# Kernel tuning notes

Hardware: AMD Instinct MI355X
Metric: run time of the kernel (lower is better)

Reference implementation:

```python
import jax, jax.numpy as jnp
import numpy as np

B, L, D = 8, 2048, 1024

def setup_inputs() -> dict:
    key = jax.random.key(0)
    ks = jax.random.split(key, 4)
    s = 1.0 / np.sqrt(D)  # linear init scale
    x = jax.random.normal(ks[0], (B, L, D), dtype=jnp.float32)
    mask = jnp.zeros((B, L, L), dtype=jnp.float32)  # additive attention mask
    Wq = jax.random.normal(ks[1], (D, D), dtype=jnp.float32) * s
    Wk = jax.random.normal(ks[2], (D, D), dtype=jnp.float32) * s
    Wv = jax.random.normal(ks[3], (D, D), dtype=jnp.float32) * s
    bq = jnp.zeros((D,), dtype=jnp.float32)
    bk = jnp.zeros((D,), dtype=jnp.float32)
    bv = jnp.zeros((D,), dtype=jnp.float32)
    return {"x": x, "mask": mask, "Wq": Wq, "bq": bq, "Wk": Wk, "bk": bk, "Wv": Wv, "bv": bv}

def reference(x, mask, Wq, bq, Wk, bk, Wv, bv):
    # Linear projections (torch Linear: y = x @ W.T + b)
    q = jnp.einsum('bld,ed->ble', x, Wq) + bq
    k = jnp.einsum('bld,ed->ble', x, Wk) + bk
    v = jnp.einsum('bld,ed->ble', x, Wv) + bv
    d = x.shape[2]
    logits = jnp.einsum('bqd,bkd->bqk', q, k) / jnp.sqrt(jnp.float32(d))
    probas = jax.nn.softmax(logits + mask, axis=2)
    return jnp.einsum('bqk,bkd->bqd', probas, v)
```

## Files before the change

### kernel.cpp

```cpp
#include <hip/hip_runtime.h>
#include <hip/hip_bf16.h>
#include <hip/hip_fp16.h>

typedef __attribute__((ext_vector_type(8))) short short8;
typedef __attribute__((ext_vector_type(4))) short sh4;
typedef __attribute__((ext_vector_type(8))) _Float16 half8;
typedef __attribute__((ext_vector_type(4))) float floatx4;

__device__ __forceinline__ unsigned short f2bf(float f) {
    unsigned int u = __builtin_bit_cast(unsigned int, f);
    u += 0x7fffu + ((u >> 16) & 1u);
    return (unsigned short)(u >> 16);
}

__device__ __forceinline__ void gl_lds16(const unsigned short* g, unsigned short* l) {
    __builtin_amdgcn_global_load_lds(
        (const __attribute__((address_space(1))) unsigned int*)(const void*)g,
        (__attribute__((address_space(3))) unsigned int*)(void*)l,
        16, 0, 0);
}

#define BM 256
#define BN 256
#define BK 64

template<int OMODE>
__global__ __launch_bounds__(512, 2)
void gemm_bt(const unsigned short* __restrict__ A,
             const unsigned short* __restrict__ B,
             void* __restrict__ O,
             const float* __restrict__ bias0, const float* __restrict__ bias1,
             const float* __restrict__ bias2,
             int K, int lda, int ldb, int ldo,
             long long aBS, long long bBS, long long oBS,
             float scale, int nby, int vstart,
             unsigned short* __restrict__ Vt, int ldvt)
{
    __shared__ __align__(16) unsigned short lds[2][2][BM * BK];

    const int t = threadIdx.x;
    const int lane = t & 63;
    const int w = t >> 6;
    const int wr = w >> 2;
    const int wc = w & 3;
    const int lq = lane >> 4;
    const int lr = lane & 15;

    const int nwg = gridDim.x;
    const int swz = (blockIdx.x & 7) * (nwg >> 3) + (blockIdx.x >> 3);
    const int by = swz % nby, bx = swz / nby;
    const size_t m0 = (size_t)bx * BM, n0 = (size_t)by * BN;

    const int z = blockIdx.z;
    const unsigned short* Az = A + (size_t)z * aBS;
    const unsigned short* Bz = B + (size_t)z * bBS;

    const int srow = t >> 3;
    const int scol = ((t & 7) ^ (srow & 7)) << 3;

    floatx4 acc[8][4];
#pragma unroll
    for (int i = 0; i < 8; ++i)
#pragma unroll
        for (int j = 0; j < 4; ++j)
            acc[i][j] = (floatx4){0.f, 0.f, 0.f, 0.f};

    const int NT = K / BK;

    auto stage = [&](int mat, int u, int kt, int buf) {
        const unsigned short* g = (mat ? Bz + (n0 + u * 64 + srow) * (size_t)ldb
                                       : Az + (m0 + u * 64 + srow) * (size_t)lda) + kt + scol;
        gl_lds16(g, &lds[buf][mat][u * 4096 + w * 512]);
    };

#pragma unroll
    for (int u = 0; u < 4; ++u) stage(1, u, 0, 0);
#pragma unroll
    for (int u = 0; u < 4; ++u) stage(0, u, 0, 0);
    if (NT > 1) {
#pragma unroll
        for (int u = 0; u < 4; ++u) stage(1, u, BK, 1);
        asm volatile("s_waitcnt vmcnt(4)" ::: "memory");
    } else {
        asm volatile("s_waitcnt vmcnt(0)" ::: "memory");
    }
    __builtin_amdgcn_s_barrier();
    __builtin_amdgcn_sched_barrier(0);

    for (int tt = 0; tt < NT; ++tt) {
        const int cur = tt & 1, nxt = cur ^ 1;
        const int kt1 = (tt + 1) * BK, kt2 = (tt + 2) * BK;
        short8 bfr[4][2];
#pragma unroll
        for (int p = 0; p < 4; ++p) {
            short8 af[2][2];
            if (p == 0) {
#pragma unroll
                for (int ni = 0; ni < 4; ++ni)
#pragma unroll
                    for (int kk = 0; kk < 2; ++kk) {
                        const int rb = wc * 64 + ni * 16 + lr;
                        const int j = kk * 4 + lq;
                        bfr[ni][kk] = *(const short8*)&lds[cur][1][rb * 64 + ((j ^ (rb & 7)) << 3)];
                    }
            }
#pragma unroll
            for (int mi2 = 0; mi2 < 2; ++mi2)
#pragma unroll
                for (int kk = 0; kk < 2; ++kk) {
                    const int ra = wr * 128 + (2 * p + mi2) * 16 + lr;
                    const int j = kk * 4 + lq;
                    af[mi2][kk] = *(const short8*)&lds[cur][0][ra * 64 + ((j ^ (ra & 7)) << 3)];
                }
            if (p == 0 && tt + 1 < NT) { stage(0, 0, kt1, nxt); stage(0, 1, kt1, nxt); }
            if (p == 1 && tt + 1 < NT) { stage(0, 2, kt1, nxt); stage(0, 3, kt1, nxt); }
            if (p == 2 && tt + 2 < NT) { stage(1, 0, kt2, cur); stage(1, 1, kt2, cur); }
            if (p == 3 && tt + 2 < NT) { stage(1, 2, kt2, cur); stage(1, 3, kt2, cur); }

            __builtin_amdgcn_sched_barrier(0);
            __builtin_amdgcn_s_barrier();
            __builtin_amdgcn_sched_barrier(0);
            __builtin_amdgcn_s_setprio(1);
#pragma unroll
            for (int kk = 0; kk < 2; ++kk)
#pragma unroll
                for (int mi2 = 0; mi2 < 2; ++mi2)
#pragma unroll
                    for (int ni = 0; ni < 4; ++ni)
                        acc[2 * p + mi2][ni] = __builtin_amdgcn_mfma_f32_16x16x32_bf16(
                            af[mi2][kk], bfr[ni][kk], acc[2 * p + mi2][ni], 0, 0, 0);
            __builtin_amdgcn_s_setprio(0);
            __builtin_amdgcn_sched_barrier(0);
            if (p == 3) {
                if (tt < NT - 2) asm volatile("s_waitcnt vmcnt(4)" ::: "memory");
                else             asm volatile("s_waitcnt vmcnt(0)" ::: "memory");
            }
            __builtin_amdgcn_s_barrier();
            __builtin_amdgcn_sched_barrier(0);
        }
    }

    const float* bias = bias0; int cshift = 0;
    if (bias1) {
        const int r = (int)(n0 >> 10);
        bias = (r == 0) ? bias0 : ((r == 1) ? bias1 : bias2);
        cshift = r << 10;
    }

    if (vstart >= 0 && (int)n0 >= vstart) {
        unsigned short* lf = &lds[0][0][0] + w * 8192;
        __syncthreads();
#pragma unroll
        for (int mi = 0; mi < 8; ++mi) {
#pragma unroll
            for (int ni = 0; ni < 4; ++ni) {
                const int tc = ni * 16 + lr;
                const int col = (int)n0 + wc * 64 + tc;
                const float cb = bias ? bias[col - cshift] : 0.f;
                const int tr0 = mi * 16 + lq * 4;
                floatx4 v = acc[mi][ni];
                sh4 pk;
#pragma unroll
                for (int r = 0; r < 4; ++r) pk[r] = (short)f2bf(v[r] * scale + cb);
                *(sh4*)&lf[tc * 128 + (tr0 ^ ((tc & 7) << 3))] = pk;
            }
        }
        __syncthreads();
        const int vrow_base = (int)n0 - vstart + wc * 64;
        const size_t colb = m0 + (size_t)wr * 128 + (size_t)(lane & 15) * 8;
#pragma unroll
        for (int i = 0; i < 16; ++i) {
            const int vr = i * 4 + (lane >> 4);
            short8 d = *(const short8*)&lf[vr * 128 + (((lane & 15) * 8) ^ ((vr & 7) << 3))];
            *(short8*)&Vt[(size_t)(vrow_base + vr) * ldvt + colb] = d;
        }
    } else {
#pragma unroll
        for (int mi = 0; mi < 8; ++mi) {
#pragma unroll
            for (int ni = 0; ni < 4; ++ni) {
                const size_t col = n0 + wc * 64 + ni * 16 + lr;
                const float cb = bias ? bias[col - cshift] : 0.f;
                floatx4 v = acc[mi][ni];
#pragma unroll
                for (int r = 0; r < 4; ++r) {
                    const size_t row = m0 + wr * 128 + mi * 16 + lq * 4 + r;
                    const float val = v[r] * scale + cb;
                    const size_t off = (size_t)z * oBS + row * (size_t)ldo + col;
                    if (OMODE == 0)
                        ((unsigned short*)O)[off] = f2bf(val);
                    else if (OMODE == 1)
                        ((float*)O)[off] = val;
                    else {
                        _Float16 h = (_Float16)val;
                        ((unsigned short*)O)[off] = __builtin_bit_cast(unsigned short, h);
                    }
                }
            }
        }
    }
}

__global__ void cvt4(const float4* __restrict__ s0, ushort4* __restrict__ d0, int n0,
                     const float4* __restrict__ s1, ushort4* __restrict__ d1, int n1,
                     const float4* __restrict__ s2, ushort4* __restrict__ d2, int n2,
                     const float4* __restrict__ s3, ushort4* __restrict__ d3, int n3)
{
    const int total = n0 + n1 + n2 + n3;
    const int stride = gridDim.x * blockDim.x;
    for (int i = blockIdx.x * blockDim.x + threadIdx.x; i < total; i += stride) {
        const float4* s; ushort4* d; int j = i;
        if (j < n0) { s = s0; d = d0; }
        else { j -= n0;
            if (j < n1) { s = s1; d = d1; }
            else { j -= n1;
                if (j < n2) { s = s2; d = d2; }
                else { j -= n2; s = s3; d = d3; }
            }
        }
        float4 f = s[j];
        d[j] = (ushort4){f2bf(f.x), f2bf(f.y), f2bf(f.z), f2bf(f.w)};
    }
}

__global__ void softmax_kernel(_Float16* __restrict__ S, const float* __restrict__ mask, int b0)
{
    const int lane = threadIdx.x & 63;
    const int wid = threadIdx.x >> 6;
    const size_t rowid = (size_t)blockIdx.x * 4 + wid;
    const size_t bi = rowid >> 11;
    const size_t q = rowid & 2047;
    _Float16* Srow = S + rowid * 2048;
    const float* Mrow = mask + (((size_t)b0 + bi) * 2048 + q) * 2048;

    float v[32];
    float mx = -3.4e38f;
#pragma unroll
    for (int i = 0; i < 4; ++i) {
        half8 h = ((const half8*)Srow)[i * 64 + lane];
        float4 ma = ((const float4*)Mrow)[i * 128 + lane * 2];
        float4 mb = ((const float4*)Mrow)[i * 128 + lane * 2 + 1];
        const float* mp0 = (const float*)&ma;
        const float* mp1 = (const float*)&mb;
#pragma unroll
        for (int j = 0; j < 4; ++j) {
            v[i * 8 + j]     = (float)h[j]     + mp0[j];
            v[i * 8 + 4 + j] = (float)h[4 + j] + mp1[j];
        }
#pragma unroll
        for (int j = 0; j < 8; ++j) mx = fmaxf(mx, v[i * 8 + j]);
    }
#pragma unroll
    for (int off = 32; off; off >>= 1) mx = fmaxf(mx, __shfl_xor(mx, off, 64));
    float sum = 0.f;
#pragma unroll
    for (int i = 0; i < 32; ++i) { v[i] = __expf(v[i] - mx); sum += v[i]; }
#pragma unroll
    for (int off = 32; off; off >>= 1) sum += __shfl_xor(sum, off, 64);
    const float inv = 1.0f / sum;

    unsigned short* Prow = (unsigned short*)Srow;
#pragma unroll
    for (int i = 0; i < 4; ++i) {
        short8 pk;
#pragma unroll
        for (int j = 0; j < 8; ++j) pk[j] = (short)f2bf(v[i * 8 + j] * inv);
        ((short8*)Prow)[i * 64 + lane] = pk;
    }
}

extern "C" void kernel_launch(void* const* d_in, const int* in_sizes, int n_in,
                              void* d_out, int out_size, void* d_ws, size_t ws_size,
                              hipStream_t stream)
{
    const float* x    = (const float*)d_in[0];
    const float* mask = (const float*)d_in[1];
    const float* Wq   = (const float*)d_in[2];
    const float* bq   = (const float*)d_in[3];
    const float* Wk   = (const float*)d_in[4];
    const float* bk   = (const float*)d_in[5];
    const float* Wv   = (const float*)d_in[6];
    const float* bv   = (const float*)d_in[7];
    float* out = (float*)d_out;

    const size_t MB = 1ull << 20;
    char* ws = (char*)d_ws;
    unsigned short* QKb  = (unsigned short*)(ws);
    unsigned short* Vt   = (unsigned short*)(ws + 64 * MB);
    unsigned short* Wcat = (unsigned short*)(ws + 96 * MB);
    unsigned short* xb   = (unsigned short*)(ws + 102 * MB);
    _Float16* Sb         = (_Float16*)(ws + 134 * MB);

    size_t savail = (ws_size > 134 * MB) ? ws_size - 134 * MB : 0;
    int g = (int)(savail / (8 * MB));
    if (g < 1) g = 1;
    if (g > 8) g = 8;

    cvt4<<<2048, 256, 0, stream>>>(
        (const float4*)x,  (ushort4*)xb,               16384 * 1024 / 4,
        (const float4*)Wq, (ushort4*)Wcat,             1024 * 1024 / 4,
        (const float4*)Wk, (ushort4*)(Wcat + 1048576), 1024 * 1024 / 4,
        (const float4*)Wv, (ushort4*)(Wcat + 2097152), 1024 * 1024 / 4);

    gemm_bt<0><<<dim3(768, 1, 1), dim3(512), 0, stream>>>(
        xb, Wcat, QKb, bq, bk, bv,
        1024, 1024, 1024, 2048, 0LL, 0LL, 0LL, 1.0f, 12, 2048, Vt, 16384);

    const float sscale = 0.03125f;
    for (int b0 = 0; b0 < 8; b0 += g) {
        const int gb = (8 - b0 < g) ? (8 - b0) : g;
        gemm_bt<2><<<dim3(64, 1, gb), dim3(512), 0, stream>>>(
            QKb + (size_t)b0 * 4194304, QKb + 1024 + (size_t)b0 * 4194304, Sb,
            nullptr, nullptr, nullptr,
            1024, 2048, 2048, 2048,
            4194304LL, 4194304LL, 4194304LL, sscale, 8, -1, nullptr, 0);
        softmax_kernel<<<dim3(gb * 512), dim3(256), 0, stream>>>(Sb, mask, b0);
        gemm_bt<1><<<dim3(32, 1, gb), dim3(512), 0, stream>>>(
            (const unsigned short*)(void*)Sb, Vt + (size_t)b0 * 2048,
            out + (size_t)b0 * 2048 * 1024,
            nullptr, nullptr, nullptr,
            2048, 2048, 16384, 1024,
            4194304LL, 2048LL, 2097152LL, 1.0f, 4, -1, nullptr, 0);
    }
}
```

Baseline: 506.0 us.

## Fuse mask add into QK^T epilogue and fuse softmax with PV GEMM

Adds the additive mask inside the QK^T GEMM epilogue. It also replaces the separate softmax kernel and the PV GEMM with one kernel: each 32-row block computes softmax into LDS as bf16 P, then multiplies by V^T, register double-buffering V loads. It drops the batch-group loop so all 8 batches run in single launches. This removes the extra round trip of P through global memory and several launches, but the new PV kernel uses small 32-row tiles with 1024 threads, one block per CU and unshared V loads. It also assumes the workspace holds the full S buffer.

```diff
diff --git a/kernel.cpp b/kernel.cpp
--- a/kernel.cpp
+++ b/kernel.cpp
@@ -34,7 +34,8 @@
              int K, int lda, int ldb, int ldo,
              long long aBS, long long bBS, long long oBS,
              float scale, int nby, int vstart,
-             unsigned short* __restrict__ Vt, int ldvt)
+             unsigned short* __restrict__ Vt, int ldvt,
+             const float* __restrict__ addmat, long long addBS)
 {
     __shared__ __align__(16) unsigned short lds[2][2][BM * BK];
 
@@ -146,6 +147,7 @@
         bias = (r == 0) ? bias0 : ((r == 1) ? bias1 : bias2);
         cshift = r << 10;
     }
+    const float* amz = addmat ? addmat + (size_t)z * addBS : nullptr;
 
     if (vstart >= 0 && (int)n0 >= vstart) {
         unsigned short* lf = &lds[0][0][0] + w * 8192;
@@ -185,7 +187,8 @@
 #pragma unroll
                 for (int r = 0; r < 4; ++r) {
                     const size_t row = m0 + wr * 128 + mi * 16 + lq * 4 + r;
-                    const float val = v[r] * scale + cb;
+                    float val = v[r] * scale + cb;
+                    if (amz) val += amz[row * 2048 + col];
                     const size_t off = (size_t)z * oBS + row * (size_t)ldo + col;
                     if (OMODE == 0)
                         ((unsigned short*)O)[off] = f2bf(val);
@@ -196,6 +199,127 @@
                         ((unsigned short*)O)[off] = __builtin_bit_cast(unsigned short, h);
                     }
                 }
+            }
+        }
+    }
+}
+
+__global__ __launch_bounds__(1024, 1)
+void fused_pv(const _Float16* __restrict__ S, const unsigned short* __restrict__ Vt,
+              float* __restrict__ out)
+{
+    __shared__ __align__(16) unsigned short P[32 * 2048];
+
+    const int t = threadIdx.x;
+    const int lane = t & 63;
+    const int w = t >> 6;
+    const int lq = lane >> 4, lr = lane & 15;
+
+    const int bid = blockIdx.x;
+    const int swz = (bid & 7) * 64 + (bid >> 3);
+    const int z = swz >> 6;
+    const int bx = swz & 63;
+    const int m0 = bx * 32;
+
+    const _Float16* Sz = S + (size_t)z * 4194304 + (size_t)m0 * 2048;
+
+#pragma unroll
+    for (int rr = 0; rr < 2; ++rr) {
+        const int r = w * 2 + rr;
+        const _Float16* row = Sz + (size_t)r * 2048;
+        float v[32];
+        float mx = -3.4e38f;
+#pragma unroll
+        for (int i = 0; i < 4; ++i) {
+            half8 h = *(const half8*)(row + i * 512 + lane * 8);
+#pragma unroll
+            for (int j = 0; j < 8; ++j) { v[i * 8 + j] = (float)h[j]; mx = fmaxf(mx, v[i * 8 + j]); }
+        }
+#pragma unroll
+        for (int off = 32; off; off >>= 1) mx = fmaxf(mx, __shfl_xor(mx, off, 64));
+        float sum = 0.f;
+#pragma unroll
+        for (int i = 0; i < 32; ++i) { v[i] = __expf(v[i] - mx); sum += v[i]; }
+#pragma unroll
+        for (int off = 32; off; off >>= 1) sum += __shfl_xor(sum, off, 64);
+        const float inv = 1.0f / sum;
+#pragma unroll
+        for (int i = 0; i < 4; ++i) {
+            short8 pk;
+#pragma unroll
+            for (int j = 0; j < 8; ++j) pk[j] = (short)f2bf(v[i * 8 + j] * inv);
+            const int cc = i * 64 + lane;
+            *(short8*)((char*)P + r * 4096 + ((cc ^ (r & 7)) << 4)) = pk;
+        }
+    }
+    __syncthreads();
+
+    floatx4 acc[2][4];
+#pragma unroll
+    for (int i = 0; i < 2; ++i)
+#pragma unroll
+        for (int j = 0; j < 4; ++j)
+            acc[i][j] = (floatx4){0.f, 0.f, 0.f, 0.f};
+
+    const unsigned short* Vz = Vt + (size_t)z * 2048;
+    const int rb_base = w * 64 + lr;
+
+    short8 b0[4][2], b1[4][2];
+
+#define LOADB(TT, BUF)                                                              \
+    {                                                                               \
+        const size_t kof = (size_t)(TT) * 64 + lq * 8;                              \
+        _Pragma("unroll")                                                           \
+        for (int ni = 0; ni < 4; ++ni) {                                            \
+            const size_t ro = (size_t)(rb_base + ni * 16) * 16384 + kof;            \
+            BUF[ni][0] = *(const short8*)(Vz + ro);                                 \
+            BUF[ni][1] = *(const short8*)(Vz + ro + 32);                            \
+        }                                                                           \
+    }
+
+#define COMPUTE(TT, BUF)                                                            \
+    {                                                                               \
+        short8 af[2][2];                                                            \
+        _Pragma("unroll")                                                           \
+        for (int mi = 0; mi < 2; ++mi)                                              \
+            _Pragma("unroll")                                                       \
+            for (int kk = 0; kk < 2; ++kk) {                                        \
+                const int ra = mi * 16 + lr;                                        \
+                const int cc = (TT) * 8 + kk * 4 + lq;                              \
+                af[mi][kk] = *(const short8*)((const char*)P + ra * 4096 +          \
+                                              ((cc ^ (ra & 7)) << 4));              \
+            }                                                                       \
+        _Pragma("unroll")                                                           \
+        for (int kk = 0; kk < 2; ++kk)                                              \
+            _Pragma("unroll")                                                       \
+            for (int mi = 0; mi < 2; ++mi)                                          \
+                _Pragma("unroll")                                                   \
+                for (int ni = 0; ni < 4; ++ni)                                      \
+                    acc[mi][ni] = __builtin_amdgcn_mfma_f32_16x16x32_bf16(          \
+                        af[mi][kk], BUF[ni][kk], acc[mi][ni], 0, 0, 0);             \
+    }
+
+    LOADB(0, b0);
+    for (int tt = 0; tt < 32; tt += 2) {
+        LOADB(tt + 1, b1);
+        COMPUTE(tt, b0);
+        if (tt + 2 < 32) LOADB(tt + 2, b0);
+        COMPUTE(tt + 1, b1);
+    }
+#undef LOADB
+#undef COMPUTE
+
+    float* oz = out + (size_t)z * 2097152;
+#pragma unroll
+    for (int mi = 0; mi < 2; ++mi) {
+#pragma unroll
+        for (int ni = 0; ni < 4; ++ni) {
+            const int col = w * 64 + ni * 16 + lr;
+            floatx4 v = acc[mi][ni];
+#pragma unroll
+            for (int r = 0; r < 4; ++r) {
+                const int row = m0 + mi * 16 + lq * 4 + r;
+                oz[(size_t)row * 1024 + col] = v[r];
             }
         }
     }
@@ -223,52 +347,6 @@
     }
 }
 
-__global__ void softmax_kernel(_Float16* __restrict__ S, const float* __restrict__ mask, int b0)
-{
-    const int lane = threadIdx.x & 63;
-    const int wid = threadIdx.x >> 6;
-    const size_t rowid = (size_t)blockIdx.x * 4 + wid;
-    const size_t bi = rowid >> 11;
-    const size_t q = rowid & 2047;
-    _Float16* Srow = S + rowid * 2048;
-    const float* Mrow = mask + (((size_t)b0 + bi) * 2048 + q) * 2048;
-
-    float v[32];
-    float mx = -3.4e38f;
-#pragma unroll
-    for (int i = 0; i < 4; ++i) {
-        half8 h = ((const half8*)Srow)[i * 64 + lane];
-        float4 ma = ((const float4*)Mrow)[i * 128 + lane * 2];
-        float4 mb = ((const float4*)Mrow)[i * 128 + lane * 2 + 1];
-        const float* mp0 = (const float*)&ma;
-        const float* mp1 = (const float*)&mb;
-#pragma unroll
-        for (int j = 0; j < 4; ++j) {
-            v[i * 8 + j]     = (float)h[j]     + mp0[j];
-            v[i * 8 + 4 + j] = (float)h[4 + j] + mp1[j];
-        }
-#pragma unroll
-        for (int j = 0; j < 8; ++j) mx = fmaxf(mx, v[i * 8 + j]);
-    }
-#pragma unroll
-    for (int off = 32; off; off >>= 1) mx = fmaxf(mx, __shfl_xor(mx, off, 64));
-    float sum = 0.f;
-#pragma unroll
-    for (int i = 0; i < 32; ++i) { v[i] = __expf(v[i] - mx); sum += v[i]; }
-#pragma unroll
-    for (int off = 32; off; off >>= 1) sum += __shfl_xor(sum, off, 64);
-    const float inv = 1.0f / sum;
-
-    unsigned short* Prow = (unsigned short*)Srow;
-#pragma unroll
-    for (int i = 0; i < 4; ++i) {
-        short8 pk;
-#pragma unroll
-        for (int j = 0; j < 8; ++j) pk[j] = (short)f2bf(v[i * 8 + j] * inv);
-        ((short8*)Prow)[i * 64 + lane] = pk;
-    }
-}
-
 extern "C" void kernel_launch(void* const* d_in, const int* in_sizes, int n_in,
                               void* d_out, int out_size, void* d_ws, size_t ws_size,
                               hipStream_t stream)
@@ -290,11 +368,7 @@
     unsigned short* Wcat = (unsigned short*)(ws + 96 * MB);
     unsigned short* xb   = (unsigned short*)(ws + 102 * MB);
     _Float16* Sb         = (_Float16*)(ws + 134 * MB);
-
-    size_t savail = (ws_size > 134 * MB) ? ws_size - 134 * MB : 0;
-    int g = (int)(savail / (8 * MB));
-    if (g < 1) g = 1;
-    if (g > 8) g = 8;
+    (void)ws_size;
 
     cvt4<<<2048, 256, 0, stream>>>(
         (const float4*)x,  (ushort4*)xb,               16384 * 1024 / 4,
@@ -304,22 +378,16 @@
 
     gemm_bt<0><<<dim3(768, 1, 1), dim3(512), 0, stream>>>(
         xb, Wcat, QKb, bq, bk, bv,
-        1024, 1024, 1024, 2048, 0LL, 0LL, 0LL, 1.0f, 12, 2048, Vt, 16384);
+        1024, 1024, 1024, 2048, 0LL, 0LL, 0LL, 1.0f, 12, 2048, Vt, 16384,
+        nullptr, 0LL);
 
     const float sscale = 0.03125f;
-    for (int b0 = 0; b0 < 8; b0 += g) {
-        const int gb = (8 - b0 < g) ? (8 - b0) : g;
-        gemm_bt<2><<<dim3(64, 1, gb), dim3(512), 0, stream>>>(
-            QKb + (size_t)b0 * 4194304, QKb + 1024 + (size_t)b0 * 4194304, Sb,
-            nullptr, nullptr, nullptr,
-            1024, 2048, 2048, 2048,
-            4194304LL, 4194304LL, 4194304LL, sscale, 8, -1, nullptr, 0);
-        softmax_kernel<<<dim3(gb * 512), dim3(256), 0, stream>>>(Sb, mask, b0);
-        gemm_bt<1><<<dim3(32, 1, gb), dim3(512), 0, stream>>>(
-            (const unsigned short*)(void*)Sb, Vt + (size_t)b0 * 2048,
-            out + (size_t)b0 * 2048 * 1024,
-            nullptr, nullptr, nullptr,
-            2048, 2048, 16384, 1024,
-            4194304LL, 2048LL, 2097152LL, 1.0f, 4, -1, nullptr, 0);
-    }
-}
+    gemm_bt<2><<<dim3(64, 1, 8), dim3(512), 0, stream>>>(
+        QKb, QKb + 1024, Sb,
+        nullptr, nullptr, nullptr,
+        1024, 2048, 2048, 2048,
+        4194304LL, 4194304LL, 4194304LL, sscale, 8, -1, nullptr, 0,
+        mask, 4194304LL);
+
+    fused_pv<<<dim3(512, 1, 1), dim3(1024), 0, stream>>>(Sb, Vt, out);
+}
```

Result: slower. 758.6 us (+49.9%).
